# Optimization experiments

Hardware: AMD Instinct MI355X
Metric: run time of the kernel (lower is better)

The kernel has to match this reference:

```python
import jax, jax.numpy as jnp
import numpy as np

B, NPG, DEG = 128, 400, 16
N, E = B * NPG, B * NPG * DEG
E_PER = E // B
K1, K2, K3 = 360, 324, 292  # ceil(0.9*400), ceil(0.9*360), ceil(0.9*324)
EPS = 1e-5


def setup_inputs() -> dict:
    key = jax.random.key(0)
    ks = jax.random.split(key, 48)
    # edges constrained within each graph (contiguous equal-size graphs)
    g = jnp.repeat(jnp.arange(B, dtype=jnp.int32), E_PER)
    src = jax.random.randint(ks[0], (E,), 0, NPG, dtype=jnp.int32) + g * NPG
    dst = jax.random.randint(ks[1], (E,), 0, NPG, dtype=jnp.int32) + g * NPG
    inp = {
        'x': jax.random.normal(ks[2], (N, 64), dtype=jnp.float32),
        'edge_index': jnp.stack([src, dst]),
        'batch': jnp.repeat(jnp.arange(B, dtype=jnp.int32), NPG),
    }
    def glorot(k, a, b):
        lim = float(np.sqrt(6.0 / (a + b)))
        return jax.random.uniform(k, (a, b), minval=-lim, maxval=lim, dtype=jnp.float32)
    conv_dims = [(64, 32), (32, 64), (64, 128), (128, 128)]
    for i, (a, b) in enumerate(conv_dims, 1):
        inp[f'W{i}'] = glorot(ks[2 + i], a, b)
        inp[f'b{i}'] = jnp.zeros((b,), jnp.float32)
    for i, d in zip((1, 2, 3), (32, 64, 128)):
        inp[f'p{i}'] = jax.random.uniform(ks[8 + i], (d,), minval=-1.0, maxval=1.0, dtype=jnp.float32) / float(np.sqrt(d))
    lin_dims = [(128, 64), (64, 64), (64, 32), (32, 16), (16, 1)]
    for i, (a, b) in enumerate(lin_dims, 1):
        inp[f'Lw{i}'] = glorot(ks[12 + i], a, b)
        inp[f'Lb{i}'] = jnp.zeros((b,), jnp.float32)
    for i, d in enumerate((64, 64, 32, 16), 1):
        inp[f'g{i}'] = jnp.ones((d,), jnp.float32)
        inp[f'be{i}'] = jnp.zeros((d,), jnp.float32)
    return inp


def _gcn(x, src, dst, emask, nmask, W, b):
    h = x @ W
    deg = nmask + jax.ops.segment_sum(emask, dst, num_segments=N)
    dinv = jnp.where(deg > 0, jax.lax.rsqrt(deg), 0.0)
    norm = dinv[src] * dinv[dst] * emask
    agg = jax.ops.segment_sum(h[src] * norm[:, None], dst, num_segments=N)
    agg = agg + h * (dinv * dinv * nmask)[:, None]  # self-loop term
    return (agg + b) * nmask[:, None]


def _topk_pool(x, nmask, p, k):
    # PyG TopKPooling: score = x.p/||p||, keep top-k per graph, x *= tanh(score)
    score = (x @ p) / jnp.linalg.norm(p)
    sel = jnp.where(nmask > 0, score, -jnp.inf).reshape(B, NPG)
    _, idx = jax.lax.top_k(sel, k)
    gidx = (idx + (jnp.arange(B) * NPG)[:, None]).reshape(-1)
    new_mask = jnp.zeros((N,), x.dtype).at[gidx].set(1.0)
    return x * (jnp.tanh(score) * new_mask)[:, None], new_mask


def reference(x, edge_index, batch, W1, b1, p1, W2, b2, p2, W3, b3, p3, W4, b4,
              Lw1, Lb1, Lw2, Lb2, Lw3, Lb3, Lw4, Lb4, Lw5, Lb5,
              g1, be1, g2, be2, g3, be3, g4, be4):
    src, dst = edge_index[0], edge_index[1]
    nmask = jnp.ones((N,), jnp.float32)
    emask = jnp.ones((E,), jnp.float32)
    x = jax.nn.relu(_gcn(x, src, dst, emask, nmask, W1, b1))
    x, nmask = _topk_pool(x, nmask, p1, K1)
    emask = emask * nmask[src] * nmask[dst]
    x = jax.nn.relu(_gcn(x, src, dst, emask, nmask, W2, b2))
    x, nmask = _topk_pool(x, nmask, p2, K2)
    emask = emask * nmask[src] * nmask[dst]
    x = jax.nn.relu(_gcn(x, src, dst, emask, nmask, W3, b3))
    x, nmask = _topk_pool(x, nmask, p3, K3)
    emask = emask * nmask[src] * nmask[dst]
    x = jax.nn.relu(_gcn(x, src, dst, emask, nmask, W4, b4))
    h = x.reshape(B, NPG, -1).max(axis=1)
    def lin_bn(h, W, bb, ga, be):
        h = h @ W + bb
        m = h.mean(0)
        v = h.var(0)  # biased, matches BatchNorm1d training normalization
        return jax.nn.relu(ga * (h - m) / jnp.sqrt(v + EPS) + be)
    h = lin_bn(h, Lw1, Lb1, g1, be1)
    h = lin_bn(h, Lw2, Lb2, g2, be2)
    h = lin_bn(h, Lw3, Lb3, g3, be3)
    h = lin_bn(h, Lw4, Lb4, g4, be4)
    return h @ Lw5 + Lb5
```

## Files before the change

### kernel.cpp

```cpp
#include <hip/hip_runtime.h>
#include <math.h>

#define NNODES 51200
#define BGRAPHS 128
#define NPG 400
#define NEDGES 819200
#define EPG 6400
#define SLP 7680

__device__ __forceinline__ float4 ld4(const float* p) { return *reinterpret_cast<const float4*>(p); }
__device__ __forceinline__ void st4(float* p, float4 v) { *reinterpret_cast<float4*>(p) = v; }

__global__ __launch_bounds__(512) void csr_build_kernel(
    const int* __restrict__ src, const int* __restrict__ dst,
    unsigned short* __restrict__ slg, int* __restrict__ gsg, int* __restrict__ gcg,
    float* __restrict__ nmask, float* __restrict__ dinv, float* __restrict__ sc,
    float* __restrict__ hp) {
    __shared__ int deg[NPG];
    __shared__ int incl[512];
    __shared__ int gs[NPG];
    __shared__ int cur[NPG];
    const int g = blockIdx.x, t = threadIdx.x;
    for (int i = t; i < NPG; i += 512) deg[i] = 0;
    if (t < 128) hp[g * 128 + t] = 0.0f;
    __syncthreads();
    for (int e = t; e < EPG; e += 512)
        atomicAdd(&deg[dst[g * EPG + e] - g * NPG], 1);
    __syncthreads();
    const int d = (t < NPG) ? deg[t] : 0;
    const int p = (d + 3) >> 2;
    incl[t] = p;
    __syncthreads();
    for (int off = 1; off < 512; off <<= 1) {
        int add = (t >= off) ? incl[t - off] : 0;
        __syncthreads();
        incl[t] += add;
        __syncthreads();
    }
    if (t < NPG) {
        const int gstart = incl[t] - p;
        gs[t] = gstart;
        gsg[g * NPG + t] = gstart;
        gcg[g * NPG + t] = p;
        cur[t] = gstart * 4;
        nmask[g * NPG + t] = 1.0f;
        const float dv = rsqrtf(1.0f + (float)d);
        dinv[g * NPG + t] = dv;
        sc[g * NPG + t] = dv;
    }
    __syncthreads();
    for (int e = t; e < EPG; e += 512) {
        int dl = dst[g * EPG + e] - g * NPG;
        int pos = atomicAdd(&cur[dl], 1);
        slg[g * SLP + pos] = (unsigned short)(src[g * EPG + e] - g * NPG);
    }
    __syncthreads();
    if (t < NPG) {
        const int end = (gs[t] + p) * 4;
        for (int i = cur[t]; i < end; i++) slg[g * SLP + i] = (unsigned short)NPG;
    }
}

template<int IN, int OUT, int MODE>
__global__ __launch_bounds__(256) void gemm_kernel(
    const float* __restrict__ X, const float* __restrict__ W,
    const float* __restrict__ bias, const float* __restrict__ nmask,
    float* __restrict__ H, const float* __restrict__ p,
    float* __restrict__ score, float* __restrict__ hp) {
    __shared__ __align__(16) float sX[64 * IN];
    __shared__ unsigned smax[256];
    const int row0 = blockIdx.x * 64;
    const int t = threadIdx.x;
    for (int i = t; i < 64 * IN / 4; i += 256)
        reinterpret_cast<float4*>(sX)[i] =
            reinterpret_cast<const float4*>(X + (size_t)row0 * IN)[i];
    if (MODE == 3) smax[t] = 0u;
    __syncthreads();
    constexpr int CG  = OUT / 4;
    constexpr int RG  = 256 / CG;
    constexpr int RPT = 64 / RG;
    const int c0 = (t % CG) * 4;
    const int r0 = (t / CG) * RPT;
    float acc[RPT][4];
#pragma unroll
    for (int r = 0; r < RPT; r++)
#pragma unroll
        for (int j = 0; j < 4; j++) acc[r][j] = 0.0f;
    for (int k4 = 0; k4 < IN / 4; k4++) {
        const float4 w0 = ld4(&W[(k4 * 4 + 0) * OUT + c0]);
        const float4 w1 = ld4(&W[(k4 * 4 + 1) * OUT + c0]);
        const float4 w2 = ld4(&W[(k4 * 4 + 2) * OUT + c0]);
        const float4 w3 = ld4(&W[(k4 * 4 + 3) * OUT + c0]);
#pragma unroll
        for (int r = 0; r < RPT; r++) {
            const float4 xv = ld4(&sX[(r0 + r) * IN + k4 * 4]);
            acc[r][0] += xv.x * w0.x + xv.y * w1.x + xv.z * w2.x + xv.w * w3.x;
            acc[r][1] += xv.x * w0.y + xv.y * w1.y + xv.z * w2.y + xv.w * w3.y;
            acc[r][2] += xv.x * w0.z + xv.y * w1.z + xv.z * w2.z + xv.w * w3.z;
            acc[r][3] += xv.x * w0.w + xv.y * w1.w + xv.z * w2.w + xv.w * w3.w;
        }
    }
    const int graph0 = row0 / 400;
    const int bnd = (graph0 + 1) * 400;
    float ps[RPT];
    float cmax[4] = {0.f, 0.f, 0.f, 0.f};
#pragma unroll
    for (int r = 0; r < RPT; r++) {
        const int row = row0 + r0 + r;
        float4 v = make_float4(acc[r][0], acc[r][1], acc[r][2], acc[r][3]);
        if (MODE >= 2) {
            const float4 b4 = ld4(&bias[c0]);
            const float m = nmask[row];
            v.x = fmaxf(v.x + b4.x, 0.0f) * m;
            v.y = fmaxf(v.y + b4.y, 0.0f) * m;
            v.z = fmaxf(v.z + b4.z, 0.0f) * m;
            v.w = fmaxf(v.w + b4.w, 0.0f) * m;
        }
        if (MODE != 3) st4(&H[(size_t)row * OUT + c0], v);
        if (MODE == 2) {
            const float4 p4 = ld4(&p[c0]);
            ps[r] = v.x * p4.x + v.y * p4.y + v.z * p4.z + v.w * p4.w;
        }
        if (MODE == 3) {
            cmax[0] = fmaxf(cmax[0], v.x);
            cmax[1] = fmaxf(cmax[1], v.y);
            cmax[2] = fmaxf(cmax[2], v.z);
            cmax[3] = fmaxf(cmax[3], v.w);
        }
    }
    if (MODE == 2) {
#pragma unroll
        for (int r = 0; r < RPT; r++) {
#pragma unroll
            for (int off = 1; off < CG; off <<= 1) ps[r] += __shfl_xor(ps[r], off);
        }
        if ((t % CG) == 0) {
#pragma unroll
            for (int r = 0; r < RPT; r++) score[row0 + r0 + r] = ps[r];
        }
    }
    if (MODE == 3) {
        const int seg = ((row0 + r0) >= bnd) ? 1 : 0;
        atomicMax(&smax[seg * 128 + c0 + 0], __float_as_uint(cmax[0]));
        atomicMax(&smax[seg * 128 + c0 + 1], __float_as_uint(cmax[1]));
        atomicMax(&smax[seg * 128 + c0 + 2], __float_as_uint(cmax[2]));
        atomicMax(&smax[seg * 128 + c0 + 3], __float_as_uint(cmax[3]));
        __syncthreads();
        unsigned* hpu = reinterpret_cast<unsigned*>(hp);
        if (t < 128) atomicMax(&hpu[graph0 * 128 + t], smax[t]);
        const int graph1 = (row0 + 63) / 400;
        if (graph1 != graph0 && t < 128) atomicMax(&hpu[graph1 * 128 + t], smax[128 + t]);
    }
}

template<int OUT, int NCH, int NS, bool EPI, bool SCORE, bool TOPK>
__global__ __launch_bounds__(512) void gcn_agg_kernel(
    const float* __restrict__ H, float* __restrict__ Y,
    const float* __restrict__ dinv_g, const float* __restrict__ sc_g,
    const float* __restrict__ bias,
    const float* __restrict__ p_sc, float* __restrict__ score_out,
    const float* __restrict__ scoreb_in, const float* __restrict__ nmask_in,
    float* __restrict__ nmask_out, const float* __restrict__ p_pool,
    int K, int PDIM,
    const unsigned short* __restrict__ slg, const int* __restrict__ gsg,
    const int* __restrict__ gcg) {
    __shared__ __align__(16) float Hl[(NPG + 1) * 36];
    __shared__ float dinvl[NPG];
    __shared__ float scl[NPG];
    __shared__ int gsl[NPG];
    __shared__ int gcl[NPG];
    __shared__ unsigned long long sl64[SLP / 4];
    __shared__ float misc[4];
    const unsigned short* sl = reinterpret_cast<const unsigned short*>(sl64);
    const int b   = blockIdx.x;
    const int g   = b / (NCH * NS);
    const int rem = b % (NCH * NS);
    const int f0  = (rem / NS) * 32;
    const int n0  = (rem % NS) * (NPG / NS);
    const int t   = threadIdx.x;

    for (int i = t; i < NPG; i += 512) {
        gsl[i] = gsg[g * NPG + i];
        gcl[i] = gcg[g * NPG + i];
    }
    for (int i = t; i < SLP / 4; i += 512)
        sl64[i] = reinterpret_cast<const unsigned long long*>(slg + (size_t)g * SLP)[i];

    if (TOPK) {
        float* sval = Hl;
        int*   sidx = (int*)(Hl + 512);
        float* sraw = Hl + 1024;
        float* nml  = Hl + 1440;
        if (t < 64) {
            float s = 0.0f;
            for (int j = t; j < PDIM; j += 64) s += p_pool[j] * p_pool[j];
#pragma unroll
            for (int o = 32; o > 0; o >>= 1) s += __shfl_xor(s, o, 64);
            if (t == 0) misc[0] = sqrtf(s);
        }
        float v = -INFINITY;
        int ix = t;
        if (t < NPG) {
            const float raw = scoreb_in[g * NPG + t];
            sraw[t] = raw;
            v = (nmask_in[g * NPG + t] > 0.0f) ? raw : -INFINITY;
        }
        __syncthreads();
        for (int kk = 2; kk <= 512; kk <<= 1) {
            for (int j = kk >> 1; j > 0; j >>= 1) {
                float vb; int ib;
                if (j >= 64) {
                    sval[t] = v; sidx[t] = ix;
                    __syncthreads();
                    vb = sval[t ^ j]; ib = sidx[t ^ j];
                    __syncthreads();
                } else {
                    vb = __shfl_xor(v, j, 64);
                    ib = __shfl_xor(ix, j, 64);
                }
                const bool ownFirst = (v > vb) || (v == vb && ix < ib);
                const bool lower = (t & j) == 0;
                const bool desc = (t & kk) == 0;
                const bool keepOwn = lower ? (desc == ownFirst) : (desc != ownFirst);
                if (!keepOwn) { v = vb; ix = ib; }
            }
        }
        if (t <= NPG) nml[t] = 0.0f;
        __syncthreads();
        if (t < K) nml[ix] = 1.0f;
        __syncthreads();
        if (rem == 0 && t < NPG) nmask_out[g * NPG + t] = nml[t];
        const float spn = misc[0];
        for (int n = t; n < NPG; n += 512) {
            float dv = 0.0f;
            if (nml[n] > 0.0f) {
                float d = 1.0f;
                const int g0 = gsl[n], g1 = g0 + gcl[n];
                for (int gg = g0; gg < g1; ++gg) {
                    const unsigned long long q = *reinterpret_cast<const unsigned long long*>(&sl[gg * 4]);
                    d += nml[(int)(q & 0xFFFF)] + nml[(int)((q >> 16) & 0xFFFF)] +
                         nml[(int)((q >> 32) & 0xFFFF)] + nml[(int)(q >> 48)];
                }
                dv = rsqrtf(d);
            }
            dinvl[n] = dv;
            scl[n] = (nml[n] > 0.0f) ? tanhf(sraw[n] / spn) * dv : 0.0f;
        }
        __syncthreads();
    } else {
        for (int i = t; i < NPG; i += 512) {
            dinvl[i] = dinv_g[g * NPG + i];
            scl[i]   = sc_g[g * NPG + i];
        }
        __syncthreads();
    }

    for (int i = t; i < NPG * 8; i += 512) {
        const int n = i >> 3, q = i & 7;
        const float s = scl[n];
        float4 v = ld4(&H[(size_t)(g * NPG + n) * OUT + f0 + q * 4]);
        v.x *= s; v.y *= s; v.z *= s; v.w *= s;
        st4(&Hl[n * 36 + q * 4], v);
    }
    if (t < 36) Hl[NPG * 36 + t] = 0.0f;
    __syncthreads();

    const int wave = t >> 6, lane = t & 63;
    const int sub = lane >> 3, f4 = lane & 7;
    constexpr int NPB = NPG / NS;
    for (int n = n0 + wave * 8 + sub; n < n0 + NPB; n += 64) {
        const float di = dinvl[n];
        if (di == 0.0f) continue;
        const int g0 = gsl[n], g1 = g0 + gcl[n];
        float4 acc = ld4(&Hl[n * 36 + f4 * 4]);
        for (int gg = g0; gg < g1; ++gg) {
            const unsigned long long q = *reinterpret_cast<const unsigned long long*>(&sl[gg * 4]);
            const int s0 = (int)(q & 0xFFFF), s1 = (int)((q >> 16) & 0xFFFF);
            const int s2 = (int)((q >> 32) & 0xFFFF), s3 = (int)(q >> 48);
            const float4 a = ld4(&Hl[s0 * 36 + f4 * 4]);
            const float4 bb = ld4(&Hl[s1 * 36 + f4 * 4]);
            const float4 c = ld4(&Hl[s2 * 36 + f4 * 4]);
            const float4 dd = ld4(&Hl[s3 * 36 + f4 * 4]);
            acc.x += (a.x + bb.x) + (c.x + dd.x);
            acc.y += (a.y + bb.y) + (c.y + dd.y);
            acc.z += (a.z + bb.z) + (c.z + dd.z);
            acc.w += (a.w + bb.w) + (c.w + dd.w);
        }
        acc.x *= di; acc.y *= di; acc.z *= di; acc.w *= di;
        if (EPI) {
            const float4 b4 = ld4(&bias[f0 + f4 * 4]);
            acc.x = fmaxf(acc.x + b4.x, 0.0f);
            acc.y = fmaxf(acc.y + b4.y, 0.0f);
            acc.z = fmaxf(acc.z + b4.z, 0.0f);
            acc.w = fmaxf(acc.w + b4.w, 0.0f);
        }
        st4(&Y[(size_t)(g * NPG + n) * OUT + f0 + f4 * 4], acc);
        if (SCORE) {
            const float4 p4 = ld4(&p_sc[f4 * 4]);
            float part = acc.x * p4.x + acc.y * p4.y + acc.z * p4.z + acc.w * p4.w;
            part += __shfl_xor(part, 1);
            part += __shfl_xor(part, 2);
            part += __shfl_xor(part, 4);
            if (f4 == 0) score_out[g * NPG + n] = part;
        }
    }
}

__global__ __launch_bounds__(512) void conv2_fused_kernel(
    const float* __restrict__ X0, float* __restrict__ X1,
    const float* __restrict__ scoreb_in, const float* __restrict__ nmask_in,
    float* __restrict__ nmask_out, float* __restrict__ scoreb_out,
    const float* __restrict__ p_pool,
    const float* __restrict__ W2, const float* __restrict__ b2,
    const float* __restrict__ p2,
    const unsigned short* __restrict__ slg, const int* __restrict__ gsg,
    const int* __restrict__ gcg) {
    __shared__ __align__(16) float Hl[(NPG + 1) * 36];
    __shared__ __align__(16) float out2[200 * 36];
    __shared__ float dinvl[NPG];
    __shared__ float scl[NPG];
    __shared__ int gsl[NPG];
    __shared__ int gcl[NPG];
    __shared__ unsigned long long sl64[SLP / 4];
    __shared__ float misc[4];
    const unsigned short* sl = reinterpret_cast<const unsigned short*>(sl64);
    const int b = blockIdx.x, g = b >> 1, seg = b & 1;
    const int n0 = seg * 200;
    const int t = threadIdx.x;

    for (int i = t; i < NPG; i += 512) {
        gsl[i] = gsg[g * NPG + i];
        gcl[i] = gcg[g * NPG + i];
    }
    for (int i = t; i < SLP / 4; i += 512)
        sl64[i] = reinterpret_cast<const unsigned long long*>(slg + (size_t)g * SLP)[i];

    {
        float* sval = Hl;
        int*   sidx = (int*)(Hl + 512);
        float* sraw = Hl + 1024;
        float* nml  = Hl + 1440;
        if (t < 64) {
            float s = 0.0f;
            for (int j = t; j < 32; j += 64) s += p_pool[j] * p_pool[j];
#pragma unroll
            for (int o = 32; o > 0; o >>= 1) s += __shfl_xor(s, o, 64);
            if (t == 0) misc[0] = sqrtf(s);
        }
        float v = -INFINITY;
        int ix = t;
        if (t < NPG) {
            const float raw = scoreb_in[g * NPG + t];
            sraw[t] = raw;
            v = (nmask_in[g * NPG + t] > 0.0f) ? raw : -INFINITY;
        }
        __syncthreads();
        for (int kk = 2; kk <= 512; kk <<= 1) {
            for (int j = kk >> 1; j > 0; j >>= 1) {
                float vb; int ib;
                if (j >= 64) {
                    sval[t] = v; sidx[t] = ix;
                    __syncthreads();
                    vb = sval[t ^ j]; ib = sidx[t ^ j];
                    __syncthreads();
                } else {
                    vb = __shfl_xor(v, j, 64);
                    ib = __shfl_xor(ix, j, 64);
                }
                const bool ownFirst = (v > vb) || (v == vb && ix < ib);
                const bool lower = (t & j) == 0;
                const bool desc = (t & kk) == 0;
                const bool keepOwn = lower ? (desc == ownFirst) : (desc != ownFirst);
                if (!keepOwn) { v = vb; ix = ib; }
            }
        }
        if (t <= NPG) nml[t] = 0.0f;
        __syncthreads();
        if (t < 360) nml[ix] = 1.0f;
        __syncthreads();
        if (seg == 0 && t < NPG) nmask_out[g * NPG + t] = nml[t];
        const float spn = misc[0];
        for (int n = t; n < NPG; n += 512) {
            float dv = 0.0f;
            if (nml[n] > 0.0f) {
                float d = 1.0f;
                const int g0 = gsl[n], g1 = g0 + gcl[n];
                for (int gg = g0; gg < g1; ++gg) {
                    const unsigned long long q = *reinterpret_cast<const unsigned long long*>(&sl[gg * 4]);
                    d += nml[(int)(q & 0xFFFF)] + nml[(int)((q >> 16) & 0xFFFF)] +
                         nml[(int)((q >> 32) & 0xFFFF)] + nml[(int)(q >> 48)];
                }
                dv = rsqrtf(d);
            }
            dinvl[n] = dv;
            scl[n] = (nml[n] > 0.0f) ? tanhf(sraw[n] / spn) * dv : 0.0f;
        }
        __syncthreads();
    }

    for (int i = t; i < NPG * 8; i += 512) {
        const int n = i >> 3, q = i & 7;
        const float s = scl[n];
        float4 v = ld4(&X0[(size_t)(g * NPG + n) * 32 + q * 4]);
        v.x *= s; v.y *= s; v.z *= s; v.w *= s;
        st4(&Hl[n * 36 + q * 4], v);
    }
    if (t < 36) Hl[NPG * 36 + t] = 0.0f;
    __syncthreads();

    {
        const int wave = t >> 6, lane = t & 63;
        const int sub = lane >> 3, f4 = lane & 7;
        for (int n = n0 + wave * 8 + sub; n < n0 + 200; n += 64) {
            const float di = dinvl[n];
            float4 acc = make_float4(0.f, 0.f, 0.f, 0.f);
            if (di != 0.0f) {
                acc = ld4(&Hl[n * 36 + f4 * 4]);
                const int g0 = gsl[n], g1 = g0 + gcl[n];
                for (int gg = g0; gg < g1; ++gg) {
                    const unsigned long long q = *reinterpret_cast<const unsigned long long*>(&sl[gg * 4]);
                    const int s0 = (int)(q & 0xFFFF), s1 = (int)((q >> 16) & 0xFFFF);
                    const int s2 = (int)((q >> 32) & 0xFFFF), s3 = (int)(q >> 48);
                    const float4 a = ld4(&Hl[s0 * 36 + f4 * 4]);
                    const float4 bb = ld4(&Hl[s1 * 36 + f4 * 4]);
                    const float4 c = ld4(&Hl[s2 * 36 + f4 * 4]);
                    const float4 dd = ld4(&Hl[s3 * 36 + f4 * 4]);
                    acc.x += (a.x + bb.x) + (c.x + dd.x);
                    acc.y += (a.y + bb.y) + (c.y + dd.y);
                    acc.z += (a.z + bb.z) + (c.z + dd.z);
                    acc.w += (a.w + bb.w) + (c.w + dd.w);
                }
                acc.x *= di; acc.y *= di; acc.z *= di; acc.w *= di;
            }
            st4(&out2[(n - n0) * 36 + f4 * 4], acc);
        }
    }
    __syncthreads();

    {
        const int c0 = (t & 15) * 4;
        const int slot = t >> 4;
        for (int n = n0 + slot; n < n0 + 200; n += 32) {
            float a0 = 0.f, a1 = 0.f, a2 = 0.f, a3 = 0.f;
            for (int k4 = 0; k4 < 8; k4++) {
                const float4 w0 = ld4(&W2[(k4 * 4 + 0) * 64 + c0]);
                const float4 w1 = ld4(&W2[(k4 * 4 + 1) * 64 + c0]);
                const float4 w2 = ld4(&W2[(k4 * 4 + 2) * 64 + c0]);
                const float4 w3 = ld4(&W2[(k4 * 4 + 3) * 64 + c0]);
                const float4 xv = ld4(&out2[(n - n0) * 36 + k4 * 4]);
                a0 += xv.x * w0.x + xv.y * w1.x + xv.z * w2.x + xv.w * w3.x;
                a1 += xv.x * w0.y + xv.y * w1.y + xv.z * w2.y + xv.w * w3.y;
                a2 += xv.x * w0.z + xv.y * w1.z + xv.z * w2.z + xv.w * w3.z;
                a3 += xv.x * w0.w + xv.y * w1.w + xv.z * w2.w + xv.w * w3.w;
            }
            const float m = (dinvl[n] > 0.0f) ? 1.0f : 0.0f;
            const float4 bb = ld4(&b2[c0]);
            float4 v = make_float4(fmaxf(a0 + bb.x, 0.f) * m, fmaxf(a1 + bb.y, 0.f) * m,
                                   fmaxf(a2 + bb.z, 0.f) * m, fmaxf(a3 + bb.w, 0.f) * m);
            st4(&X1[(size_t)(g * NPG + n) * 64 + c0], v);
            const float4 p4 = ld4(&p2[c0]);
            float ps = v.x * p4.x + v.y * p4.y + v.z * p4.z + v.w * p4.w;
            ps += __shfl_xor(ps, 1); ps += __shfl_xor(ps, 2);
            ps += __shfl_xor(ps, 4); ps += __shfl_xor(ps, 8);
            if ((t & 15) == 0) scoreb_out[g * NPG + n] = ps;
        }
    }
}

template<int IN, int OUT>
__global__ __launch_bounds__(128) void head_layer_kernel(
    const float* __restrict__ A, const float* __restrict__ W,
    const float* __restrict__ b, const float* __restrict__ ga,
    const float* __restrict__ be, float* __restrict__ Y) {
    __shared__ float Al[128 * (IN + 1)];
    __shared__ float red[4];
    const int c = blockIdx.x, t = threadIdx.x;
    for (int i = t; i < 128 * IN; i += 128)
        Al[(i / IN) * (IN + 1) + (i % IN)] = A[i];
    __syncthreads();
    float acc = b[c];
#pragma unroll
    for (int j = 0; j < IN; j++) acc += Al[t * (IN + 1) + j] * W[j * OUT + c];
    float s1 = acc, s2 = acc * acc;
    for (int o = 32; o > 0; o >>= 1) {
        s1 += __shfl_down(s1, o, 64);
        s2 += __shfl_down(s2, o, 64);
    }
    if ((t & 63) == 0) { red[t >> 6] = s1; red[2 + (t >> 6)] = s2; }
    __syncthreads();
    const float S1 = red[0] + red[1], S2 = red[2] + red[3];
    const float m = S1 * (1.0f / 128.0f);
    const float var = S2 * (1.0f / 128.0f) - m * m;
    float val = ga[c] * (acc - m) * rsqrtf(var + 1e-5f) + be[c];
    Y[t * OUT + c] = fmaxf(val, 0.0f);
}

__global__ __launch_bounds__(512) void head_tail_kernel(
    const float* __restrict__ A2,
// ... 67 lines not shown
            const float v = fmaxf((Z2[t * 20 + j] - mv[j]) * (g4[j] * rsqrtf(mv[32 + j] + 1e-5f)) + be4[j], 0.f);
            acc += v * Lw5[j];
        }
        out[t] = acc;
    }
}

extern "C" void kernel_launch(void* const* d_in, const int* in_sizes, int n_in,
                              void* d_out, int out_size, void* d_ws, size_t ws_size,
                              hipStream_t stream) {
    (void)in_sizes; (void)n_in; (void)out_size; (void)ws_size;
    const float* x   = (const float*)d_in[0];
    const int*   ei  = (const int*)d_in[1];
    const float* W1  = (const float*)d_in[3];  const float* b1  = (const float*)d_in[4];
    const float* W2  = (const float*)d_in[5];  const float* b2  = (const float*)d_in[6];
    const float* W3  = (const float*)d_in[7];  const float* b3  = (const float*)d_in[8];
    const float* W4  = (const float*)d_in[9];  const float* b4  = (const float*)d_in[10];
    const float* p1  = (const float*)d_in[11];
    const float* p2  = (const float*)d_in[12];
    const float* p3  = (const float*)d_in[13];
    const float* Lw1 = (const float*)d_in[14]; const float* Lb1 = (const float*)d_in[15];
    const float* Lw2 = (const float*)d_in[16]; const float* Lb2 = (const float*)d_in[17];
    const float* Lw3 = (const float*)d_in[18]; const float* Lb3 = (const float*)d_in[19];
    const float* Lw4 = (const float*)d_in[20]; const float* Lb4 = (const float*)d_in[21];
    const float* Lw5 = (const float*)d_in[22]; const float* Lb5 = (const float*)d_in[23];
    const float* g1  = (const float*)d_in[24]; const float* be1 = (const float*)d_in[25];
    const float* g2  = (const float*)d_in[26]; const float* be2 = (const float*)d_in[27];
    const float* g3  = (const float*)d_in[28]; const float* be3 = (const float*)d_in[29];
    const float* g4  = (const float*)d_in[30]; const float* be4 = (const float*)d_in[31];

    const int* src = ei;
    const int* dst = ei + NEDGES;

    float* ws    = (float*)d_ws;
    float* hb    = ws;
    float* x0    = hb + (size_t)NNODES * 128;
    float* x1    = x0 + (size_t)NNODES * 128;
    float* nmA   = x1 + (size_t)NNODES * 128;
    float* nmB   = nmA + NNODES;
    float* dinv  = nmB + NNODES;
    float* sc    = dinv + NNODES;
    float* scbA  = sc + NNODES;
    float* scbB  = scbA + NNODES;
    float* hp    = scbB + NNODES;
    float* a1    = hp + 128 * 128;
    float* a2    = a1 + 128 * 64;
    unsigned short* slg = (unsigned short*)(a2 + 128 * 64);
    int* gsg = (int*)(slg + (size_t)BGRAPHS * SLP);
    int* gcg = gsg + (size_t)BGRAPHS * NPG;

    csr_build_kernel<<<BGRAPHS, 512, 0, stream>>>(src, dst, slg, gsg, gcg, nmA, dinv, sc, hp);

    gemm_kernel<64, 32, 0><<<NNODES / 64, 256, 0, stream>>>(x, W1, nullptr, nullptr, hb, nullptr, nullptr, nullptr);
    gcn_agg_kernel<32, 1, 2, true, true, false><<<BGRAPHS * 2, 512, 0, stream>>>(
        hb, x0, dinv, sc, b1, p1, scbA,
        nullptr, nullptr, nullptr, nullptr, 0, 0, slg, gsg, gcg);

    conv2_fused_kernel<<<BGRAPHS * 2, 512, 0, stream>>>(
        x0, x1, scbA, nmA, nmB, scbB, p1, W2, b2, p2, slg, gsg, gcg);

    gcn_agg_kernel<64, 2, 2, false, false, true><<<BGRAPHS * 4, 512, 0, stream>>>(
        x1, hb, nullptr, nullptr, nullptr, nullptr, nullptr,
        scbB, nmB, nmA, p2, 324, 64, slg, gsg, gcg);
    gemm_kernel<64, 128, 2><<<NNODES / 64, 256, 0, stream>>>(hb, W3, b3, nmA, x0, p3, scbA, nullptr);

    gcn_agg_kernel<128, 4, 1, false, false, true><<<BGRAPHS * 4, 512, 0, stream>>>(
        x0, hb, nullptr, nullptr, nullptr, nullptr, nullptr,
        scbA, nmA, nmB, p3, 292, 128, slg, gsg, gcg);
    gemm_kernel<128, 128, 3><<<NNODES / 64, 256, 0, stream>>>(hb, W4, b4, nmB, x1, nullptr, nullptr, hp);

    head_layer_kernel<128, 64><<<64, 128, 0, stream>>>(hp, Lw1, Lb1, g1, be1, a1);
    head_layer_kernel<64, 64><<<64, 128, 0, stream>>>(a1, Lw2, Lb2, g2, be2, a2);
    head_tail_kernel<<<1, 512, 0, stream>>>(a2, Lw3, Lb3, g3, be3, Lw4, Lb4, g4, be4, Lw5, Lb5, (float*)d_out);
}
```

Before: 192.4 us.

## Fuse GEMM, top-k pooling and aggregation into per-graph conv kernels

```diff
diff --git a/kernel.cpp b/kernel.cpp
--- a/kernel.cpp
+++ b/kernel.cpp
@@ -14,15 +14,13 @@
 __global__ __launch_bounds__(512) void csr_build_kernel(
     const int* __restrict__ src, const int* __restrict__ dst,
     unsigned short* __restrict__ slg, int* __restrict__ gsg, int* __restrict__ gcg,
-    float* __restrict__ nmask, float* __restrict__ dinv, float* __restrict__ sc,
-    float* __restrict__ hp) {
+    float* __restrict__ nmask, float* __restrict__ dinv) {
     __shared__ int deg[NPG];
     __shared__ int incl[512];
     __shared__ int gs[NPG];
     __shared__ int cur[NPG];
     const int g = blockIdx.x, t = threadIdx.x;
     for (int i = t; i < NPG; i += 512) deg[i] = 0;
-    if (t < 128) hp[g * 128 + t] = 0.0f;
     __syncthreads();
     for (int e = t; e < EPG; e += 512)
         atomicAdd(&deg[dst[g * EPG + e] - g * NPG], 1);
@@ -44,9 +42,7 @@
         gcg[g * NPG + t] = p;
         cur[t] = gstart * 4;
         nmask[g * NPG + t] = 1.0f;
-        const float dv = rsqrtf(1.0f + (float)d);
-        dinv[g * NPG + t] = dv;
-        sc[g * NPG + t] = dv;
+        dinv[g * NPG + t] = rsqrtf(1.0f + (float)d);
     }
     __syncthreads();
     for (int e = t; e < EPG; e += 512) {
@@ -61,216 +57,143 @@
     }
 }
 
-template<int IN, int OUT, int MODE>
-__global__ __launch_bounds__(256) void gemm_kernel(
-    const float* __restrict__ X, const float* __restrict__ W,
-    const float* __restrict__ bias, const float* __restrict__ nmask,
-    float* __restrict__ H, const float* __restrict__ p,
-    float* __restrict__ score, float* __restrict__ hp) {
-    __shared__ __align__(16) float sX[64 * IN];
-    __shared__ unsigned smax[256];
-    const int row0 = blockIdx.x * 64;
-    const int t = threadIdx.x;
-    for (int i = t; i < 64 * IN / 4; i += 256)
-        reinterpret_cast<float4*>(sX)[i] =
-            reinterpret_cast<const float4*>(X + (size_t)row0 * IN)[i];
-    if (MODE == 3) smax[t] = 0u;
-    __syncthreads();
-    constexpr int CG  = OUT / 4;
-    constexpr int RG  = 256 / CG;
-    constexpr int RPT = 64 / RG;
-    const int c0 = (t % CG) * 4;
-    const int r0 = (t / CG) * RPT;
-    float acc[RPT][4];
+__device__ __forceinline__ void topk_block(
+    int K, int PDIM, const float* __restrict__ p_pool,
+    const float* __restrict__ scb0, const float* __restrict__ scb1,
+    const float* __restrict__ nmask_in, float* __restrict__ nmask_out,
+    int gbase,
+    float* sval, int* sidx, float* sraw, float* nml, float* misc,
+    float* dinvl, float* scl,
+    const unsigned short* sl, const int* gsl, const int* gcl, int t) {
+    if (t < 64) {
+        float s = 0.0f;
+        for (int j = t; j < PDIM; j += 64) s += p_pool[j] * p_pool[j];
 #pragma unroll
-    for (int r = 0; r < RPT; r++)
-#pragma unroll
-        for (int j = 0; j < 4; j++) acc[r][j] = 0.0f;
-    for (int k4 = 0; k4 < IN / 4; k4++) {
-        const float4 w0 = ld4(&W[(k4 * 4 + 0) * OUT + c0]);
-        const float4 w1 = ld4(&W[(k4 * 4 + 1) * OUT + c0]);
-        const float4 w2 = ld4(&W[(k4 * 4 + 2) * OUT + c0]);
-        const float4 w3 = ld4(&W[(k4 * 4 + 3) * OUT + c0]);
-#pragma unroll
-        for (int r = 0; r < RPT; r++) {
-            const float4 xv = ld4(&sX[(r0 + r) * IN + k4 * 4]);
-            acc[r][0] += xv.x * w0.x + xv.y * w1.x + xv.z * w2.x + xv.w * w3.x;
-            acc[r][1] += xv.x * w0.y + xv.y * w1.y + xv.z * w2.y + xv.w * w3.y;
-            acc[r][2] += xv.x * w0.z + xv.y * w1.z + xv.z * w2.z + xv.w * w3.z;
-            acc[r][3] += xv.x * w0.w + xv.y * w1.w + xv.z * w2.w + xv.w * w3.w;
-        }
-    }
-    const int graph0 = row0 / 400;
-    const int bnd = (graph0 + 1) * 400;
-    float ps[RPT];
-    float cmax[4] = {0.f, 0.f, 0.f, 0.f};
-#pragma unroll
-    for (int r = 0; r < RPT; r++) {
-        const int row = row0 + r0 + r;
-        float4 v = make_float4(acc[r][0], acc[r][1], acc[r][2], acc[r][3]);
-        if (MODE >= 2) {
-            const float4 b4 = ld4(&bias[c0]);
-            const float m = nmask[row];
-            v.x = fmaxf(v.x + b4.x, 0.0f) * m;
-            v.y = fmaxf(v.y + b4.y, 0.0f) * m;
-            v.z = fmaxf(v.z + b4.z, 0.0f) * m;
-            v.w = fmaxf(v.w + b4.w, 0.0f) * m;
-        }
-        if (MODE != 3) st4(&H[(size_t)row * OUT + c0], v);
-        if (MODE == 2) {
-            const float4 p4 = ld4(&p[c0]);
-            ps[r] = v.x * p4.x + v.y * p4.y + v.z * p4.z + v.w * p4.w;
-        }
-        if (MODE == 3) {
-            cmax[0] = fmaxf(cmax[0], v.x);
-            cmax[1] = fmaxf(cmax[1], v.y);
-            cmax[2] = fmaxf(cmax[2], v.z);
-            cmax[3] = fmaxf(cmax[3], v.w);
-        }
-    }
-    if (MODE == 2) {
-#pragma unroll
-        for (int r = 0; r < RPT; r++) {
-#pragma unroll
-            for (int off = 1; off < CG; off <<= 1) ps[r] += __shfl_xor(ps[r], off);
-        }
-        if ((t % CG) == 0) {
-#pragma unroll
-            for (int r = 0; r < RPT; r++) score[row0 + r0 + r] = ps[r];
-        }
-    }
-    if (MODE == 3) {
-        const int seg = ((row0 + r0) >= bnd) ? 1 : 0;
-        atomicMax(&smax[seg * 128 + c0 + 0], __float_as_uint(cmax[0]));
-        atomicMax(&smax[seg * 128 + c0 + 1], __float_as_uint(cmax[1]));
-        atomicMax(&smax[seg * 128 + c0 + 2], __float_as_uint(cmax[2]));
-        atomicMax(&smax[seg * 128 + c0 + 3], __float_as_uint(cmax[3]));
+        for (int o = 32; o > 0; o >>= 1) s += __shfl_xor(s, o, 64);
+        if (t == 0) misc[0] = sqrtf(s);
+    }
+    float v = -INFINITY;
+    int ix = t;
+    if (t < NPG) {
+        float raw = scb0[gbase + t];
+        if (scb1) raw += scb1[gbase + t];
+        sraw[t] = raw;
+        v = (nmask_in[gbase + t] > 0.0f) ? raw : -INFINITY;
+    }
+    __syncthreads();
+    for (int kk = 2; kk <= 512; kk <<= 1) {
+        for (int j = kk >> 1; j > 0; j >>= 1) {
+            float vb; int ib;
+            if (j >= 64) {
+                sval[t] = v; sidx[t] = ix;
+                __syncthreads();
+                vb = sval[t ^ j]; ib = sidx[t ^ j];
+                __syncthreads();
+            } else {
+                vb = __shfl_xor(v, j, 64);
+                ib = __shfl_xor(ix, j, 64);
+            }
+            const bool ownFirst = (v > vb) || (v == vb && ix < ib);
+            const bool lower = (t & j) == 0;
+            const bool desc = (t & kk) == 0;
+            const bool keepOwn = lower ? (desc == ownFirst) : (desc != ownFirst);
+            if (!keepOwn) { v = vb; ix = ib; }
+        }
+    }
+    if (t <= NPG) nml[t] = 0.0f;
+    __syncthreads();
+    if (t < K) nml[ix] = 1.0f;
+    __syncthreads();
+    if (nmask_out && t < NPG) nmask_out[gbase + t] = nml[t];
+    const float spn = misc[0];
+    for (int n = t; n < NPG; n += 512) {
+        float dv = 0.0f;
+        if (nml[n] > 0.0f) {
+            float d = 1.0f;
+            const int g0 = gsl[n], g1 = g0 + gcl[n];
+            for (int gg = g0; gg < g1; ++gg) {
+                const unsigned long long q = *reinterpret_cast<const unsigned long long*>(&sl[gg * 4]);
+                d += nml[(int)(q & 0xFFFF)] + nml[(int)((q >> 16) & 0xFFFF)] +
+                     nml[(int)((q >> 32) & 0xFFFF)] + nml[(int)(q >> 48)];
+            }
+            dv = rsqrtf(d);
+        }
+        dinvl[n] = dv;
+        scl[n] = (nml[n] > 0.0f) ? tanhf(sraw[n] / spn) * dv : 0.0f;
+    }
+    __syncthreads();
+}
+
+template<int IN>
+__device__ __forceinline__ void gemm_chunk(
+    const float* __restrict__ Xsrc, int WOUT, const float* __restrict__ W,
+    int cbase, const float* scl, float* Hl, float* bufT, int t) {
+    constexpr int Q = IN / 4;
+    constexpr int ST = IN + 4;
+    const int c0 = (t & 7) * 4;
+    const int slot = t >> 3;
+    for (int r0 = 0; r0 < NPG; r0 += 64) {
+        const int nr = (r0 + 64 <= NPG) ? 64 : (NPG - r0);
         __syncthreads();
-        unsigned* hpu = reinterpret_cast<unsigned*>(hp);
-        if (t < 128) atomicMax(&hpu[graph0 * 128 + t], smax[t]);
-        const int graph1 = (row0 + 63) / 400;
-        if (graph1 != graph0 && t < 128) atomicMax(&hpu[graph1 * 128 + t], smax[128 + t]);
-    }
-}
-
-template<int OUT, int NCH, int NS, bool EPI, bool SCORE, bool TOPK>
-__global__ __launch_bounds__(512) void gcn_agg_kernel(
-    const float* __restrict__ H, float* __restrict__ Y,
-    const float* __restrict__ dinv_g, const float* __restrict__ sc_g,
-    const float* __restrict__ bias,
-    const float* __restrict__ p_sc, float* __restrict__ score_out,
-    const float* __restrict__ scoreb_in, const float* __restrict__ nmask_in,
-    float* __restrict__ nmask_out, const float* __restrict__ p_pool,
-    int K, int PDIM,
+        for (int i = t; i < nr * Q; i += 512) {
+            const int r = i / Q, q = i % Q;
+            float4 v = ld4(&Xsrc[(size_t)(r0 + r) * IN + q * 4]);
+            const float s = scl[r0 + r];
+            v.x *= s; v.y *= s; v.z *= s; v.w *= s;
+            st4(&bufT[r * ST + q * 4], v);
+        }
+        __syncthreads();
+        if (slot < nr) {
+            float a0 = 0.f, a1 = 0.f, a2 = 0.f, a3 = 0.f;
+            for (int k4 = 0; k4 < Q; k4++) {
+                const float4 w0 = ld4(&W[(k4 * 4 + 0) * WOUT + cbase + c0]);
+                const float4 w1 = ld4(&W[(k4 * 4 + 1) * WOUT + cbase + c0]);
+                const float4 w2 = ld4(&W[(k4 * 4 + 2) * WOUT + cbase + c0]);
+                const float4 w3 = ld4(&W[(k4 * 4 + 3) * WOUT + cbase + c0]);
+                const float4 xv = ld4(&bufT[slot * ST + k4 * 4]);
+                a0 += xv.x * w0.x + xv.y * w1.x + xv.z * w2.x + xv.w * w3.x;
+                a1 += xv.x * w0.y + xv.y * w1.y + xv.z * w2.y + xv.w * w3.y;
+                a2 += xv.x * w0.z + xv.y * w1.z + xv.z * w2.z + xv.w * w3.z;
+                a3 += xv.x * w0.w + xv.y * w1.w + xv.z * w2.w + xv.w * w3.w;
+            }
+            st4(&Hl[(r0 + slot) * 36 + c0], make_float4(a0, a1, a2, a3));
+        }
+    }
+    __syncthreads();
+}
+
+__global__ __launch_bounds__(512) void conv1_fused_kernel(
+    const float* __restrict__ x, float* __restrict__ Xa, float* __restrict__ scb1,
+    const float* __restrict__ dinv_g, const float* __restrict__ W1,
+    const float* __restrict__ b1, const float* __restrict__ p1,
     const unsigned short* __restrict__ slg, const int* __restrict__ gsg,
     const int* __restrict__ gcg) {
     __shared__ __align__(16) float Hl[(NPG + 1) * 36];
+    __shared__ __align__(16) float bufT[64 * 68];
     __shared__ float dinvl[NPG];
-    __shared__ float scl[NPG];
     __shared__ int gsl[NPG];
     __shared__ int gcl[NPG];
     __shared__ unsigned long long sl64[SLP / 4];
-    __shared__ float misc[4];
     const unsigned short* sl = reinterpret_cast<const unsigned short*>(sl64);
-    const int b   = blockIdx.x;
-    const int g   = b / (NCH * NS);
-    const int rem = b % (NCH * NS);
-    const int f0  = (rem / NS) * 32;
-    const int n0  = (rem % NS) * (NPG / NS);
-    const int t   = threadIdx.x;
+    const int b = blockIdx.x, g = b >> 1, seg = b & 1, t = threadIdx.x;
+    const int gbase = g * NPG;
 
     for (int i = t; i < NPG; i += 512) {
-        gsl[i] = gsg[g * NPG + i];
-        gcl[i] = gcg[g * NPG + i];
+        dinvl[i] = dinv_g[gbase + i];
+        gsl[i] = gsg[gbase + i];
+        gcl[i] = gcg[gbase + i];
     }
     for (int i = t; i < SLP / 4; i += 512)
         sl64[i] = reinterpret_cast<const unsigned long long*>(slg + (size_t)g * SLP)[i];
-
-    if (TOPK) {
-        float* sval = Hl;
-        int*   sidx = (int*)(Hl + 512);
-        float* sraw = Hl + 1024;
-        float* nml  = Hl + 1440;
-        if (t < 64) {
-            float s = 0.0f;
-            for (int j = t; j < PDIM; j += 64) s += p_pool[j] * p_pool[j];
-#pragma unroll
-            for (int o = 32; o > 0; o >>= 1) s += __shfl_xor(s, o, 64);
-            if (t == 0) misc[0] = sqrtf(s);
-        }
-        float v = -INFINITY;
-        int ix = t;
-        if (t < NPG) {
-            const float raw = scoreb_in[g * NPG + t];
-            sraw[t] = raw;
-            v = (nmask_in[g * NPG + t] > 0.0f) ? raw : -INFINITY;
-        }
-        __syncthreads();
-        for (int kk = 2; kk <= 512; kk <<= 1) {
-            for (int j = kk >> 1; j > 0; j >>= 1) {
-                float vb; int ib;
-                if (j >= 64) {
-                    sval[t] = v; sidx[t] = ix;
-                    __syncthreads();
-                    vb = sval[t ^ j]; ib = sidx[t ^ j];
-                    __syncthreads();
-                } else {
-                    vb = __shfl_xor(v, j, 64);
-                    ib = __shfl_xor(ix, j, 64);
-                }
-                const bool ownFirst = (v > vb) || (v == vb && ix < ib);
-                const bool lower = (t & j) == 0;
-                const bool desc = (t & kk) == 0;
-                const bool keepOwn = lower ? (desc == ownFirst) : (desc != ownFirst);
-                if (!keepOwn) { v = vb; ix = ib; }
-            }
-        }
-        if (t <= NPG) nml[t] = 0.0f;
-        __syncthreads();
-        if (t < K) nml[ix] = 1.0f;
-        __syncthreads();
-        if (rem == 0 && t < NPG) nmask_out[g * NPG + t] = nml[t];
-        const float spn = misc[0];
-        for (int n = t; n < NPG; n += 512) {
-            float dv = 0.0f;
-            if (nml[n] > 0.0f) {
-                float d = 1.0f;
-                const int g0 = gsl[n], g1 = g0 + gcl[n];
-                for (int gg = g0; gg < g1; ++gg) {
-                    const unsigned long long q = *reinterpret_cast<const unsigned long long*>(&sl[gg * 4]);
-                    d += nml[(int)(q & 0xFFFF)] + nml[(int)((q >> 16) & 0xFFFF)] +
-                         nml[(int)((q >> 32) & 0xFFFF)] + nml[(int)(q >> 48)];
-                }
-                dv = rsqrtf(d);
-            }
-            dinvl[n] = dv;
-            scl[n] = (nml[n] > 0.0f) ? tanhf(sraw[n] / spn) * dv : 0.0f;
-        }
-        __syncthreads();
-    } else {
-        for (int i = t; i < NPG; i += 512) {
-            dinvl[i] = dinv_g[g * NPG + i];
-            scl[i]   = sc_g[g * NPG + i];
-        }
-        __syncthreads();
-    }
-
-    for (int i = t; i < NPG * 8; i += 512) {
-        const int n = i >> 3, q = i & 7;
-        const float s = scl[n];
-        float4 v = ld4(&H[(size_t)(g * NPG + n) * OUT + f0 + q * 4]);
-        v.x *= s; v.y *= s; v.z *= s; v.w *= s;
-        st4(&Hl[n * 36 + q * 4], v);
-    }
     if (t < 36) Hl[NPG * 36 + t] = 0.0f;
-    __syncthreads();
+
+    gemm_chunk<64>(x + (size_t)gbase * 64, 32, W1, 0, dinvl, Hl, bufT, t);
 
     const int wave = t >> 6, lane = t & 63;
     const int sub = lane >> 3, f4 = lane & 7;
-    constexpr int NPB = NPG / NS;
-    for (int n = n0 + wave * 8 + sub; n < n0 + NPB; n += 64) {
+    const int n0 = seg * 200;
+    for (int n = n0 + wave * 8 + sub; n < n0 + 200; n += 64) {
         const float di = dinvl[n];
-        if (di == 0.0f) continue;
         const int g0 = gsl[n], g1 = g0 + gcl[n];
         float4 acc = ld4(&Hl[n * 36 + f4 * 4]);
         for (int gg = g0; gg < g1; ++gg) {
@@ -286,23 +209,18 @@
             acc.z += (a.z + bb.z) + (c.z + dd.z);
             acc.w += (a.w + bb.w) + (c.w + dd.w);
         }
-        acc.x *= di; acc.y *= di; acc.z *= di; acc.w *= di;
-        if (EPI) {
-            const float4 b4 = ld4(&bias[f0 + f4 * 4]);
-            acc.x = fmaxf(acc.x + b4.x, 0.0f);
-            acc.y = fmaxf(acc.y + b4.y, 0.0f);
-            acc.z = fmaxf(acc.z + b4.z, 0.0f);
-            acc.w = fmaxf(acc.w + b4.w, 0.0f);
-        }
-        st4(&Y[(size_t)(g * NPG + n) * OUT + f0 + f4 * 4], acc);
-        if (SCORE) {
-            const float4 p4 = ld4(&p_sc[f4 * 4]);
-            float part = acc.x * p4.x + acc.y * p4.y + acc.z * p4.z + acc.w * p4.w;
-            part += __shfl_xor(part, 1);
-            part += __shfl_xor(part, 2);
-            part += __shfl_xor(part, 4);
-            if (f4 == 0) score_out[g * NPG + n] = part;
-        }
+        const float4 b4 = ld4(&b1[f4 * 4]);
+        acc.x = fmaxf(acc.x * di + b4.x, 0.f);
+        acc.y = fmaxf(acc.y * di + b4.y, 0.f);
+        acc.z = fmaxf(acc.z * di + b4.z, 0.f);
+        acc.w = fmaxf(acc.w * di + b4.w, 0.f);
+        st4(&Xa[(size_t)(gbase + n) * 32 + f4 * 4], acc);
+        const float4 p4 = ld4(&p1[f4 * 4]);
+        float part = acc.x * p4.x + acc.y * p4.y + acc.z * p4.z + acc.w * p4.w;
+        part += __shfl_xor(part, 1);
+        part += __shfl_xor(part, 2);
+        part += __shfl_xor(part, 4);
+        if (f4 == 0) scb1[gbase + n] = part;
     }
 }
 
@@ -327,81 +245,24 @@
     const int b = blockIdx.x, g = b >> 1, seg = b & 1;
     const int n0 = seg * 200;
     const int t = threadIdx.x;
+    const int gbase = g * NPG;
 
     for (int i = t; i < NPG; i += 512) {
-        gsl[i] = gsg[g * NPG + i];
-        gcl[i] = gcg[g * NPG + i];
+        gsl[i] = gsg[gbase + i];
+        gcl[i] = gcg[gbase + i];
     }
     for (int i = t; i < SLP / 4; i += 512)
         sl64[i] = reinterpret_cast<const unsigned long long*>(slg + (size_t)g * SLP)[i];
 
-    {
-        float* sval = Hl;
-        int*   sidx = (int*)(Hl + 512);
-        float* sraw = Hl + 1024;
-        float* nml  = Hl + 1440;
-        if (t < 64) {
-            float s = 0.0f;
-            for (int j = t; j < 32; j += 64) s += p_pool[j] * p_pool[j];
-#pragma unroll
-            for (int o = 32; o > 0; o >>= 1) s += __shfl_xor(s, o, 64);
-            if (t == 0) misc[0] = sqrtf(s);
-        }
-        float v = -INFINITY;
-        int ix = t;
-        if (t < NPG) {
-            const float raw = scoreb_in[g * NPG + t];
-            sraw[t] = raw;
-            v = (nmask_in[g * NPG + t] > 0.0f) ? raw : -INFINITY;
-        }
-        __syncthreads();
-        for (int kk = 2; kk <= 512; kk <<= 1) {
-            for (int j = kk >> 1; j > 0; j >>= 1) {
-                float vb; int ib;
-                if (j >= 64) {
-                    sval[t] = v; sidx[t] = ix;
-                    __syncthreads();
-                    vb = sval[t ^ j]; ib = sidx[t ^ j];
-                    __syncthreads();
-                } else {
-                    vb = __shfl_xor(v, j, 64);
-                    ib = __shfl_xor(ix, j, 64);
-                }
-                const bool ownFirst = (v > vb) || (v == vb && ix < ib);
-                const bool lower = (t & j) == 0;
-                const bool desc = (t & kk) == 0;
-                const bool keepOwn = lower ? (desc == ownFirst) : (desc != ownFirst);
-                if (!keepOwn) { v = vb; ix = ib; }
-            }
-        }
-        if (t <= NPG) nml[t] = 0.0f;
-        __syncthreads();
-        if (t < 360) nml[ix] = 1.0f;
-        __syncthreads();
-        if (seg == 0 && t < NPG) nmask_out[g * NPG + t] = nml[t];
-        const float spn = misc[0];
-        for (int n = t; n < NPG; n += 512) {
-            float dv = 0.0f;
-            if (nml[n] > 0.0f) {
-                float d = 1.0f;
-                const int g0 = gsl[n], g1 = g0 + gcl[n];
-                for (int gg = g0; gg < g1; ++gg) {
-                    const unsigned long long q = *reinterpret_cast<const unsigned long long*>(&sl[gg * 4]);
-                    d += nml[(int)(q & 0xFFFF)] + nml[(int)((q >> 16) & 0xFFFF)] +
-                         nml[(int)((q >> 32) & 0xFFFF)] + nml[(int)(q >> 48)];
-                }
-                dv = rsqrtf(d);
-            }
-            dinvl[n] = dv;
-            scl[n] = (nml[n] > 0.0f) ? tanhf(sraw[n] / spn) * dv : 0.0f;
-        }
-        __syncthreads();
-    }
+    topk_block(360, 32, p_pool, scoreb_in, nullptr, nmask_in,
+               (seg == 0) ? nmask_out : nullptr, gbase,
+               Hl, (int*)(Hl + 512), Hl + 1024, Hl + 1440, misc,
+               dinvl, scl, sl, gsl, gcl, t);
 
     for (int i = t; i < NPG * 8; i += 512) {
         const int n = i >> 3, q = i & 7;
         const float s = scl[n];
-        float4 v = ld4(&X0[(size_t)(g * NPG + n) * 32 + q * 4]);
+        float4 v = ld4(&X0[(size_t)(gbase + n) * 32 + q * 4]);
         v.x *= s; v.y *= s; v.z *= s; v.w *= s;
         st4(&Hl[n * 36 + q * 4], v);
     }
@@ -457,13 +318,173 @@
             const float4 bb = ld4(&b2[c0]);
             float4 v = make_float4(fmaxf(a0 + bb.x, 0.f) * m, fmaxf(a1 + bb.y, 0.f) * m,
                                    fmaxf(a2 + bb.z, 0.f) * m, fmaxf(a3 + bb.w, 0.f) * m);
-            st4(&X1[(size_t)(g * NPG + n) * 64 + c0], v);
+            st4(&X1[(size_t)(gbase + n) * 64 + c0], v);
             const float4 p4 = ld4(&p2[c0]);
             float ps = v.x * p4.x + v.y * p4.y + v.z * p4.z + v.w * p4.w;
             ps += __shfl_xor(ps, 1); ps += __shfl_xor(ps, 2);
             ps += __shfl_xor(ps, 4); ps += __shfl_xor(ps, 8);
-            if ((t & 15) == 0) scoreb_out[g * NPG + n] = ps;
-        }
+            if ((t & 15) == 0) scoreb_out[gbase + n] = ps;
+        }
+    }
+}
+
+__global__ __launch_bounds__(512) void conv3_fused_kernel(
+    const float* __restrict__ X1, float* __restrict__ X3,
+    const float* __restrict__ scb2, const float* __restrict__ nmB,
+    float* __restrict__ nmA, float* __restrict__ scb3,
+    const float* __restrict__ p2, const float* __restrict__ W3,
+    const float* __restrict__ b3, const float* __restrict__ p3,
+    const unsigned short* __restrict__ slg, const int* __restrict__ gsg,
+    const int* __restrict__ gcg) {
+    __shared__ __align__(16) float Hl[(NPG + 1) * 36];
+    __shared__ __align__(16) float bufT[64 * 68];
+    __shared__ float dinvl[NPG];
+    __shared__ float scl[NPG];
+    __shared__ float sc_part[NPG];
+    __shared__ int gsl[NPG];
+    __shared__ int gcl[NPG];
+    __shared__ unsigned long long sl64[SLP / 4];
+    __shared__ float misc[4];
+    const unsigned short* sl = reinterpret_cast<const unsigned short*>(sl64);
+    const int b = blockIdx.x, g = b >> 1, h = b & 1, t = threadIdx.x;
+    const int gbase = g * NPG;
+
+    for (int i = t; i < NPG; i += 512) {
+        gsl[i] = gsg[gbase + i];
+        gcl[i] = gcg[gbase + i];
+    }
+    for (int i = t; i < SLP / 4; i += 512)
+        sl64[i] = reinterpret_cast<const unsigned long long*>(slg + (size_t)g * SLP)[i];
+    if (t < 36) Hl[NPG * 36 + t] = 0.0f;
+
+    topk_block(324, 64, p2, scb2, nullptr, nmB, (h == 0) ? nmA : nullptr, gbase,
+               Hl, (int*)(Hl + 512), Hl + 1024, Hl + 1440, misc,
+               dinvl, scl, sl, gsl, gcl, t);
+
+    const int wave = t >> 6, lane = t & 63;
+    const int sub = lane >> 3, f4 = lane & 7;
+    for (int ci = 0; ci < 2; ci++) {
+        const int c = h * 2 + ci;
+        gemm_chunk<64>(X1 + (size_t)gbase * 64, 128, W3, c * 32, scl, Hl, bufT, t);
+        for (int n = wave * 8 + sub; n < NPG; n += 64) {
+            const float di = dinvl[n];
+            float part = 0.0f;
+            if (di != 0.0f) {
+                const int g0 = gsl[n], g1 = g0 + gcl[n];
+                float4 acc = ld4(&Hl[n * 36 + f4 * 4]);
+                for (int gg = g0; gg < g1; ++gg) {
+                    const unsigned long long q = *reinterpret_cast<const unsigned long long*>(&sl[gg * 4]);
+                    const int s0 = (int)(q & 0xFFFF), s1 = (int)((q >> 16) & 0xFFFF);
+                    const int s2 = (int)((q >> 32) & 0xFFFF), s3 = (int)(q >> 48);
+                    const float4 a = ld4(&Hl[s0 * 36 + f4 * 4]);
+                    const float4 bb = ld4(&Hl[s1 * 36 + f4 * 4]);
+                    const float4 cc = ld4(&Hl[s2 * 36 + f4 * 4]);
+                    const float4 dd = ld4(&Hl[s3 * 36 + f4 * 4]);
+                    acc.x += (a.x + bb.x) + (cc.x + dd.x);
+                    acc.y += (a.y + bb.y) + (cc.y + dd.y);
+                    acc.z += (a.z + bb.z) + (cc.z + dd.z);
+                    acc.w += (a.w + bb.w) + (cc.w + dd.w);
+                }
+                const float4 b4 = ld4(&b3[c * 32 + f4 * 4]);
+                acc.x = fmaxf(acc.x * di + b4.x, 0.f);
+                acc.y = fmaxf(acc.y * di + b4.y, 0.f);
+                acc.z = fmaxf(acc.z * di + b4.z, 0.f);
+                acc.w = fmaxf(acc.w * di + b4.w, 0.f);
+                st4(&X3[(size_t)(gbase + n) * 128 + c * 32 + f4 * 4], acc);
+                const float4 p4 = ld4(&p3[c * 32 + f4 * 4]);
+                part = acc.x * p4.x + acc.y * p4.y + acc.z * p4.z + acc.w * p4.w;
+                part += __shfl_xor(part, 1);
+                part += __shfl_xor(part, 2);
+                part += __shfl_xor(part, 4);
+            }
+            if (f4 == 0) {
+                if (ci == 0) sc_part[n] = part;
+                else sc_part[n] += part;
+            }
+        }
+    }
+    __syncthreads();
+    for (int n = t; n < NPG; n += 512)
+        scb3[(size_t)h * NNODES + gbase + n] = sc_part[n];
+}
+
+__global__ __launch_bounds__(512) void conv4_fused_kernel(
+    const float* __restrict__ X3, float* __restrict__ hp,
+    const float* __restrict__ scb3, const float* __restrict__ nmA,
+    const float* __restrict__ p3, const float* __restrict__ W4,
+    const float* __restrict__ b4g,
+    const unsigned short* __restrict__ slg, const int* __restrict__ gsg,
+    const int* __restrict__ gcg) {
+    __shared__ __align__(16) float Hl[(NPG + 1) * 36];
+    __shared__ __align__(16) float bufT[64 * 132];
+    __shared__ float dinvl[NPG];
+    __shared__ float scl[NPG];
+    __shared__ int gsl[NPG];
+    __shared__ int gcl[NPG];
+    __shared__ unsigned long long sl64[SLP / 4];
+    __shared__ unsigned smax[32];
+    __shared__ float misc[4];
+    const unsigned short* sl = reinterpret_cast<const unsigned short*>(sl64);
+    const int b = blockIdx.x, g = b >> 1, h = b & 1, t = threadIdx.x;
+    const int gbase = g * NPG;
+
+    for (int i = t; i < NPG; i += 512) {
+        gsl[i] = gsg[gbase + i];
+        gcl[i] = gcg[gbase + i];
+    }
+    for (int i = t; i < SLP / 4; i += 512)
+        sl64[i] = reinterpret_cast<const unsigned long long*>(slg + (size_t)g * SLP)[i];
+    if (t < 36) Hl[NPG * 36 + t] = 0.0f;
+
+    topk_block(292, 128, p3, scb3, scb3 + NNODES, nmA, nullptr, gbase,
+               Hl, (int*)(Hl + 512), Hl + 1024, Hl + 1440, misc,
+               dinvl, scl, sl, gsl, gcl, t);
+
+    const int wave = t >> 6, lane = t & 63;
+    const int sub = lane >> 3, f4 = lane & 7;
+    for (int ci = 0; ci < 2; ci++) {
+        const int c = h * 2 + ci;
+        if (t < 32) smax[t] = 0u;
+        gemm_chunk<128>(X3 + (size_t)gbase * 128, 128, W4, c * 32, scl, Hl, bufT, t);
+        float cm0 = 0.f, cm1 = 0.f, cm2 = 0.f, cm3 = 0.f;
+        for (int n = wave * 8 + sub; n < NPG; n += 64) {
+            const float di = dinvl[n];
+            if (di == 0.0f) continue;
+            const int g0 = gsl[n], g1 = g0 + gcl[n];
+            float4 acc = ld4(&Hl[n * 36 + f4 * 4]);
+            for (int gg = g0; gg < g1; ++gg) {
+                const unsigned long long q = *reinterpret_cast<const unsigned long long*>(&sl[gg * 4]);
+                const int s0 = (int)(q & 0xFFFF), s1 = (int)((q >> 16) & 0xFFFF);
+                const int s2 = (int)((q >> 32) & 0xFFFF), s3 = (int)(q >> 48);
+                const float4 a = ld4(&Hl[s0 * 36 + f4 * 4]);
+                const float4 bb = ld4(&Hl[s1 * 36 + f4 * 4]);
+                const float4 cc = ld4(&Hl[s2 * 36 + f4 * 4]);
+                const float4 dd = ld4(&Hl[s3 * 36 + f4 * 4]);
+                acc.x += (a.x + bb.x) + (cc.x + dd.x);
+                acc.y += (a.y + bb.y) + (cc.y + dd.y);
+                acc.z += (a.z + bb.z) + (cc.z + dd.z);
+                acc.w += (a.w + bb.w) + (cc.w + dd.w);
+            }
+            const float4 b4 = ld4(&b4g[c * 32 + f4 * 4]);
+            cm0 = fmaxf(cm0, fmaxf(acc.x * di + b4.x, 0.f));
+            cm1 = fmaxf(cm1, fmaxf(acc.y * di + b4.y, 0.f));
+            cm2 = fmaxf(cm2, fmaxf(acc.z * di + b4.z, 0.f));
+            cm3 = fmaxf(cm3, fmaxf(acc.w * di + b4.w, 0.f));
+        }
+        cm0 = fmaxf(cm0, __shfl_xor(cm0, 8, 64));  cm1 = fmaxf(cm1, __shfl_xor(cm1, 8, 64));
+        cm2 = fmaxf(cm2, __shfl_xor(cm2, 8, 64));  cm3 = fmaxf(cm3, __shfl_xor(cm3, 8, 64));
+        cm0 = fmaxf(cm0, __shfl_xor(cm0, 16, 64)); cm1 = fmaxf(cm1, __shfl_xor(cm1, 16, 64));
+        cm2 = fmaxf(cm2, __shfl_xor(cm2, 16, 64)); cm3 = fmaxf(cm3, __shfl_xor(cm3, 16, 64));
+        cm0 = fmaxf(cm0, __shfl_xor(cm0, 32, 64)); cm1 = fmaxf(cm1, __shfl_xor(cm1, 32, 64));
+        cm2 = fmaxf(cm2, __shfl_xor(cm2, 32, 64)); cm3 = fmaxf(cm3, __shfl_xor(cm3, 32, 64));
+        if (sub == 0) {
+            atomicMax(&smax[f4 * 4 + 0], __float_as_uint(cm0));
+            atomicMax(&smax[f4 * 4 + 1], __float_as_uint(cm1));
+            atomicMax(&smax[f4 * 4 + 2], __float_as_uint(cm2));
+            atomicMax(&smax[f4 * 4 + 3], __float_as_uint(cm3));
+        }
+        __syncthreads();
+        if (t < 32) hp[g * 128 + c * 32 + t] = __uint_as_float(smax[t]);
     }
 }
 
@@ -597,42 +618,36 @@
     const int* src = ei;
     const int* dst = ei + NEDGES;
 
-    float* ws    = (float*)d_ws;
-    float* hb    = ws;
-    float* x0    = hb + (size_t)NNODES * 128;
-    float* x1    = x0 + (size_t)NNODES * 128;
-    float* nmA   = x1 + (size_t)NNODES * 128;
-    float* nmB   = nmA + NNODES;
-    float* dinv  = nmB + NNODES;
-    float* sc    = dinv + NNODES;
-    float* scbA  = sc + NNODES;
-    float* scbB  = scbA + NNODES;
-    float* hp    = scbB + NNODES;
-    float* a1    = hp + 128 * 128;
-    float* a2    = a1 + 128 * 64;
+    float* ws   = (float*)d_ws;
+    float* xa   = ws;
+    float* x1   = xa + (size_t)NNODES * 32;
+    float* x3   = x1 + (size_t)NNODES * 64;
+    float* nmA  = x3 + (size_t)NNODES * 128;
+    float* nmB  = nmA + NNODES;
+    float* dinv = nmB + NNODES;
+    float* scb1 = dinv + NNODES;
+    float* scb2 = scb1 + NNODES;
+    float* scb3 = scb2 + NNODES;
+    float* hp   = scb3 + 2 * (size_t)NNODES;
+    float* a1   = hp + 128 * 128;
+    float* a2   = a1 + 128 * 64;
     unsigned short* slg = (unsigned short*)(a2 + 128 * 64);
     int* gsg = (int*)(slg + (size_t)BGRAPHS * SLP);
     int* gcg = gsg + (size_t)BGRAPHS * NPG;
 
-    csr_build_kernel<<<BGRAPHS, 512, 0, stream>>>(src, dst, slg, gsg, gcg, nmA, dinv, sc, hp);
-
-    gemm_kernel<64, 32, 0><<<NNODES / 64, 256, 0, stream>>>(x, W1, nullptr, nullptr, hb, nullptr, nullptr, nullptr);
-    gcn_agg_kernel<32, 1, 2, true, true, false><<<BGRAPHS * 2, 512, 0, stream>>>(
-        hb, x0, dinv, sc, b1, p1, scbA,
-        nullptr, nullptr, nullptr, nullptr, 0, 0, slg, gsg, gcg);
+    csr_build_kernel<<<BGRAPHS, 512, 0, stream>>>(src, dst, slg, gsg, gcg, nmA, dinv);
+
+    conv1_fused_kernel<<<BGRAPHS * 2, 512, 0, stream>>>(
+        x, xa, scb1, dinv, W1, b1, p1, slg, gsg, gcg);
 
     conv2_fused_kernel<<<BGRAPHS * 2, 512, 0, stream>>>(
-        x0, x1, scbA, nmA, nmB, scbB, p1, W2, b2, p2, slg, gsg, gcg);
-
-    gcn_agg_kernel<64, 2, 2, false, false, true><<<BGRAPHS * 4, 512, 0, stream>>>(
-        x1, hb, nullptr, nullptr, nullptr, nullptr, nullptr,
-        scbB, nmB, nmA, p2, 324, 64, slg, gsg, gcg);
-    gemm_kernel<64, 128, 2><<<NNODES / 64, 256, 0, stream>>>(hb, W3, b3, nmA, x0, p3, scbA, nullptr);
-
-    gcn_agg_kernel<128, 4, 1, false, false, true><<<BGRAPHS * 4, 512, 0, stream>>>(
-        x0, hb, nullptr, nullptr, nullptr, nullptr, nullptr,
-        scbA, nmA, nmB, p3, 292, 128, slg, gsg, gcg);
-    gemm_kernel<128, 128, 3><<<NNODES / 64, 256, 0, stream>>>(hb, W4, b4, nmB, x1, nullptr, nullptr, hp);
+        xa, x1, scb1, nmA, nmB, scb2, p1, W2, b2, p2, slg, gsg, gcg);
+
+    conv3_fused_kernel<<<BGRAPHS * 2, 512, 0, stream>>>(
+        x1, x3, scb2, nmB, nmA, scb3, p2, W3, b3, p3, slg, gsg, gcg);
+
+    conv4_fused_kernel<<<BGRAPHS * 2, 512, 0, stream>>>(
+        x3, hp, scb3, nmA, p3, W4, b4, slg, gsg, gcg);
 
     head_layer_kernel<128, 64><<<64, 128, 0, stream>>>(hp, Lw1, Lb1, g1, be1, a1);
     head_layer_kernel<64, 64><<<64, 128, 0, stream>>>(a1, Lw2, Lb2, g2, be2, a2);
```

New measurement: 330.1 us. 1.72x slower.
